# Kernel optimization log

Hardware: AMD Instinct MI355X
Metric: run time of the kernel (lower is better)

Reference implementation:

```python
import jax, jax.numpy as jnp
import numpy as np

D_MODEL = 2048
D_STATE = 16
D_CONV = 4
EXPAND = 2
D_INNER = EXPAND * D_MODEL  # 4096
DT_RANK = 128               # ceil(2048/16)
BATCH = 2
SEQ = 1024


def setup_inputs() -> dict:
    key = jax.random.key(0)
    ks = jax.random.split(key, 10)
    n = lambda k, shape, scale: jax.random.normal(k, shape, dtype=jnp.float32) * scale
    # A_log = log(arange(1..N)) broadcast over channels, exactly as in the torch init
    A_log = jnp.log(jnp.tile(jnp.arange(1, D_STATE + 1, dtype=jnp.float32)[None, :], (D_INNER, 1)))
    return {
        "hidden_states": n(ks[0], (BATCH, SEQ, D_MODEL), 1.0),
        "W_in": n(ks[1], (2 * D_INNER, D_MODEL), 0.02),
        "conv_w": n(ks[2], (D_INNER, D_CONV), 0.2),
        "conv_b": n(ks[3], (D_INNER,), 0.02),
        "W_x": n(ks[4], (DT_RANK + 2 * D_STATE, D_INNER), 0.02),
        "W_dt": n(ks[5], (D_INNER, DT_RANK), 0.05),
        "b_dt": n(ks[6], (D_INNER,), 0.5) - 4.0,  # softplus(b_dt) ~ small dt, like inv-softplus init
        "A_log": A_log,
        "D_skip": jnp.ones((D_INNER,), jnp.float32),
        "W_out": n(ks[7], (D_MODEL, D_INNER), 0.02),
    }


def _mamba_forward(hidden_states, W_in, conv_w, conv_b, W_x, W_dt, b_dt, A_log, D_skip, W_out):
    B, L, _ = hidden_states.shape
    # in_proj then split into x (SSM path) and z (gate)
    xz = hidden_states @ W_in.T                      # (B, L, 2*Di)
    x, z = jnp.split(xz, 2, axis=-1)                 # (B, L, Di) each
    # causal depthwise conv1d (kernel D_CONV, left pad D_CONV-1) + SiLU
    xp = jnp.pad(x, ((0, 0), (D_CONV - 1, 0), (0, 0)))
    xc = conv_b
    for k in range(D_CONV):
        xc = xc + conv_w[:, k] * xp[:, k:k + L, :]
    x = jax.nn.silu(xc)                              # (B, L, Di)
    # input-dependent dt, B, C
    x_dbl = x @ W_x.T                                # (B, L, dt_rank + 2N)
    dt_low, B_in, C_in = jnp.split(x_dbl, [DT_RANK, DT_RANK + D_STATE], axis=-1)
    dt = dt_low @ W_dt.T                             # (B, L, Di); bias added inside scan (delta_bias)
    delta = jax.nn.softplus(dt + b_dt)               # (B, L, Di)
    A = -jnp.exp(A_log)                              # (Di, N)

    def step(h, inp):
        delta_t, u_t, B_t, C_t = inp                 # (B,Di),(B,Di),(B,N),(B,N)
        dA = jnp.exp(delta_t[..., None] * A)         # (B, Di, N)
        h = dA * h + (delta_t * u_t)[..., None] * B_t[:, None, :]
        y_t = jnp.einsum('bdn,bn->bd', h, C_t)
        return h, y_t

    h0 = jnp.zeros((B, D_INNER, D_STATE), x.dtype)
    xs = (jnp.swapaxes(delta, 0, 1), jnp.swapaxes(x, 0, 1),
          jnp.swapaxes(B_in, 0, 1), jnp.swapaxes(C_in, 0, 1))
    _, ys = jax.lax.scan(step, h0, xs)               # ys: (L, B, Di)
    y = jnp.swapaxes(ys, 0, 1)                       # (B, L, Di)
    y = y + D_skip * x                               # skip connection
    y = y * jax.nn.silu(z)                           # output gating
    return y @ W_out.T                               # (B, L, D_MODEL)


def reference(hidden_states, W_in, conv_w, conv_b, W_x, W_dt, b_dt, A_log, D_skip, W_out):
    return _mamba_forward(hidden_states, W_in, conv_w, conv_b, W_x, W_dt, b_dt, A_log, D_skip, W_out)
```

## Files before the change

### kernel.cpp

```cpp
#include <hip/hip_runtime.h>
#include <hip/hip_bf16.h>


#define BATCH 2
#define SEQ 1024
#define DMODEL 2048
#define DINNER 4096
#define DSTATE 16
#define DTRANK 128
#define ROWS (BATCH * SEQ)
#define XDBL_N (DTRANK + 2 * DSTATE)
#define NCHUNK 64
#define CLEN (SEQ / NCHUNK)
#define WXPAD 192

typedef unsigned short ushort_t;
typedef __attribute__((ext_vector_type(8))) short short8;
typedef __attribute__((ext_vector_type(4))) float f32x4;

__device__ __forceinline__ ushort_t bf16_rne(float f) {
  unsigned u = __float_as_uint(f);
  return (ushort_t)((u + 0x7FFFu + ((u >> 16) & 1u)) >> 16);
}

__global__ __launch_bounds__(256) void cast_bf16(
    const float* __restrict__ x, ushort_t* __restrict__ o, int n4) {
  int i = blockIdx.x * 256 + threadIdx.x;
  if (i >= n4) return;
  float4 v = ((const float4*)x)[i];
  ushort4 h;
  h.x = bf16_rne(v.x); h.y = bf16_rne(v.y);
  h.z = bf16_rne(v.z); h.w = bf16_rne(v.w);
  ((ushort4*)o)[i] = h;
}

__global__ __launch_bounds__(256) void cast_wx(
    const float* __restrict__ wx, ushort_t* __restrict__ o) {
  int i = blockIdx.x * 256 + threadIdx.x;
  if (i >= WXPAD * (DINNER / 4)) return;
  int row = i >> 10;
  ushort4 h = {0, 0, 0, 0};
  if (row < XDBL_N) {
    float4 v = ((const float4*)wx)[i];
    h.x = bf16_rne(v.x); h.y = bf16_rne(v.y);
    h.z = bf16_rne(v.z); h.w = bf16_rne(v.w);
  }
  ((ushort4*)o)[i] = h;
}

template <int TM, int TN, int EPI, bool SK>
__global__ __launch_bounds__(256, 2) void gemm_bf16(
    const ushort_t* __restrict__ X, int lda,
    const ushort_t* __restrict__ W, int ldb,
    const float* __restrict__ bias,
    float* __restrict__ C, int ldc, int kslice, size_t sstride) {
  constexpr int MI = TM / 32;
  constexpr int NI = TN / 32;
  constexpr int G = (TM + TN) / 32;
  __shared__ __attribute__((aligned(16))) ushort_t lds[(TM + TN) * 64];

  const int tid = threadIdx.x;
  const int lane = tid & 63;
  const int w = tid >> 6;
  const int wm = w & 1, wn = w >> 1;
  const int m0 = blockIdx.x * TM;
  const int n0 = blockIdx.y * TN;
  const int kbase = SK ? blockIdx.z * kslice : 0;

  const int lrow = lane >> 3;
  const int csw = (lane & 7) ^ lrow;
  const int quad = lane >> 4;
  const int l15 = lane & 15;
  const int x0 = quad ^ (lane & 7);
  const int baseA = (wm * (TM / 2) + l15) * 64;
  const int baseB = (TM + wn * (TN / 2) + l15) * 64;

  f32x4 acc[MI][NI] = {};

  for (int kt = 0; kt < kslice; kt += 64) {
#pragma unroll
    for (int j = 0; j < G; j++) {
      const int r0 = (w * G + j) * 8;
      const int row = r0 + lrow;
      const ushort_t* src = (r0 < TM)
          ? X + (size_t)(m0 + row) * lda + kbase + kt + csw * 8
          : W + (size_t)(n0 + row - TM) * ldb + kbase + kt + csw * 8;
      __builtin_amdgcn_global_load_lds(
          (const __attribute__((address_space(1))) unsigned int*)src,
          (__attribute__((address_space(3))) unsigned int*)&lds[r0 * 64],
          16, 0, 0);
    }
    __syncthreads();

#pragma unroll
    for (int ks = 0; ks < 2; ks++) {
      const int xo = (x0 ^ (ks * 4)) * 8;
      short8 a[MI], b[NI];
#pragma unroll
      for (int mi = 0; mi < MI; mi++)
        a[mi] = *(const short8*)&lds[baseA + mi * 1024 + xo];
#pragma unroll
      for (int ni = 0; ni < NI; ni++)
        b[ni] = *(const short8*)&lds[baseB + ni * 1024 + xo];
#pragma unroll
      for (int mi = 0; mi < MI; mi++)
#pragma unroll
        for (int ni = 0; ni < NI; ni++)
          acc[mi][ni] = __builtin_amdgcn_mfma_f32_16x16x32_bf16(
              a[mi], b[ni], acc[mi][ni], 0, 0, 0);
    }
    __syncthreads();
  }

  float* Cs = SK ? (C + (size_t)blockIdx.z * sstride) : C;
#pragma unroll
  for (int mi = 0; mi < MI; mi++)
#pragma unroll
    for (int ni = 0; ni < NI; ni++) {
      int row = m0 + wm * (TM / 2) + mi * 16 + quad * 4;
      int col = n0 + wn * (TN / 2) + ni * 16 + l15;
#pragma unroll
      for (int r = 0; r < 4; r++) {
        float v = acc[mi][ni][r];
        if (EPI == 1) {
          v += bias[col];
          v = (v > 20.f) ? v : log1pf(__expf(v));
        }
        Cs[(size_t)(row + r) * ldc + col] = v;
      }
    }
}

__global__ __launch_bounds__(192) void reduce8(
    const float* __restrict__ partials, float* __restrict__ xdbl,
    ushort_t* __restrict__ dtb) {
  int m = blockIdx.x;
  int c = threadIdx.x;
  if (c >= XDBL_N) return;
  float s = 0.f;
#pragma unroll
  for (int z = 0; z < 8; z++)
    s += partials[(size_t)z * ROWS * WXPAD + (size_t)m * WXPAD + c];
  xdbl[(size_t)m * XDBL_N + c] = s;
  if (c < DTRANK) dtb[(size_t)m * DTRANK + c] = bf16_rne(s);
}

__global__ __launch_bounds__(256) void conv_silu(
    const float* __restrict__ xz, const float* __restrict__ cw,
    const float* __restrict__ cb, float* __restrict__ xs,
    ushort_t* __restrict__ xsb) {
  int idx = blockIdx.x * 256 + threadIdx.x;
  if (idx >= ROWS * DINNER) return;
  int d = idx & (DINNER - 1);
  int bt = idx >> 12;
  int t = bt & (SEQ - 1);
  float acc = cb[d];
#pragma unroll
  for (int k = 0; k < 4; k++) {
    int tt = t - 3 + k;
    if (tt >= 0) acc += cw[d * 4 + k] * xz[(size_t)(bt - 3 + k) * (2 * DINNER) + d];
  }
  float s = acc / (1.f + __expf(-acc));
  xs[idx] = s;
  xsb[idx] = bf16_rne(s);
}

__global__ __launch_bounds__(256) void scan_pass1(
    const float* __restrict__ delta, const float* __restrict__ xs,
    const float* __restrict__ xdbl, const float* __restrict__ A_log,
    float* __restrict__ hpart, float* __restrict__ sumd) {
  int g = blockIdx.x * 256 + threadIdx.x;
  int d = g & (DINNER - 1);
  int rest = g >> 12;
  int c = rest & (NCHUNK - 1);
  int b = rest >> 6;

  float Adn[16];
#pragma unroll
  for (int q = 0; q < 4; q++) {
    float4 a = *(const float4*)&A_log[d * 16 + q * 4];
    Adn[q * 4 + 0] = -__expf(a.x); Adn[q * 4 + 1] = -__expf(a.y);
    Adn[q * 4 + 2] = -__expf(a.z); Adn[q * 4 + 3] = -__expf(a.w);
  }

  float h[16] = {};
  float sd = 0.f;
  const size_t t0 = (size_t)b * SEQ + c * CLEN;
  const float* dp = delta + t0 * DINNER + d;
  const float* up = xs + t0 * DINNER + d;
  const float* xb = xdbl + t0 * XDBL_N + DTRANK;

  for (int i = 0; i < CLEN; i++) {
    float dt = dp[(size_t)i * DINNER];
    float u = up[(size_t)i * DINNER];
    sd += dt;
    float du = dt * u;
    float Bv[16];
#pragma unroll
    for (int q = 0; q < 4; q++)
      *(float4*)&Bv[q * 4] = *(const float4*)&xb[i * XDBL_N + q * 4];
#pragma unroll
    for (int n = 0; n < 16; n++)
      h[n] = __expf(dt * Adn[n]) * h[n] + du * Bv[n];
  }

  float* hp = hpart + ((size_t)(c * BATCH + b) * DINNER + d) * 16;
#pragma unroll
  for (int q = 0; q < 4; q++) *(float4*)&hp[q * 4] = *(const float4*)&h[q * 4];
  sumd[(size_t)(c * BATCH + b) * DINNER + d] = sd;
}

__global__ __launch_bounds__(256) void scan_pass2(
    float* __restrict__ hph, const float* __restrict__ sumd,
    const float* __restrict__ A_log) {
  int g = blockIdx.x * 256 + threadIdx.x;
  int n = g & 15;
  int d = (g >> 4) & (DINNER - 1);
  int b = g >> 16;

  float Adn = -__expf(A_log[d * 16 + n]);
  float h = 0.f;
  for (int c = 0; c < NCHUNK; c++) {
    size_t base = (size_t)(c * BATCH + b) * DINNER + d;
    float part = hph[base * 16 + n];
    hph[base * 16 + n] = h;
    h = __expf(Adn * sumd[base]) * h + part;
  }
}

__global__ __launch_bounds__(256) void scan_pass3(
    const float* __restrict__ xz, const float* __restrict__ xs,
    const float* __restrict__ xdbl, const float* __restrict__ A_log,
    const float* __restrict__ D_skip, const float* __restrict__ h0,
    const float* __restrict__ delta, ushort_t* __restrict__ gated) {
  int g = blockIdx.x * 256 + threadIdx.x;
  int d = g & (DINNER - 1);
  int rest = g >> 12;
  int c = rest & (NCHUNK - 1);
  int b = rest >> 6;

  float Adn[16];
#pragma unroll
  for (int q = 0; q < 4; q++) {
    float4 a = *(const float4*)&A_log[d * 16 + q * 4];
    Adn[q * 4 + 0] = -__expf(a.x); Adn[q * 4 + 1] = -__expf(a.y);
    Adn[q * 4 + 2] = -__expf(a.z); Adn[q * 4 + 3] = -__expf(a.w);
  }
  float Dd = D_skip[d];

  float h[16];
  const float* hp = h0 + ((size_t)(c * BATCH + b) * DINNER + d) * 16;
#pragma unroll
  for (int q = 0; q < 4; q++) *(float4*)&h[q * 4] = *(const float4*)&hp[q * 4];

  const size_t t0 = (size_t)b * SEQ + c * CLEN;
  const float* dl = delta + t0 * DINNER + d;
  const float* up = xs + t0 * DINNER + d;
  const float* zb = xz + t0 * (2 * DINNER) + DINNER + d;
  const float* xb = xdbl + t0 * XDBL_N + DTRANK;
  ushort_t* gp = gated + t0 * DINNER + d;

  for (int i = 0; i < CLEN; i++) {
    float dt = dl[(size_t)i * DINNER];
    float u = up[(size_t)i * DINNER];
    float du = dt * u;
    float Bv[16], Cv[16];
#pragma unroll
    for (int q = 0; q < 4; q++) {
      *(float4*)&Bv[q * 4] = *(const float4*)&xb[i * XDBL_N + q * 4];
      *(float4*)&Cv[q * 4] = *(const float4*)&xb[i * XDBL_N + DSTATE + q * 4];
    }
    float y = 0.f;
#pragma unroll
    for (int n = 0; n < 16; n++) {
      h[n] = __expf(dt * Adn[n]) * h[n] + du * Bv[n];
      y += h[n] * Cv[n];
    }
    float z = zb[(size_t)i * (2 * DINNER)];
    float sz = z / (1.f + __expf(-z));
    gp[(size_t)i * DINNER] = bf16_rne((y + Dd * u) * sz);
  }
}

extern "C" void kernel_launch(void* const* d_in, const int* in_sizes, int n_in,
                              void* d_out, int out_size, void* d_ws, size_t ws_size,
                              hipStream_t stream) {
  const float* hidden = (const float*)d_in[0];
  const float* W_in   = (const float*)d_in[1];
  const float* conv_w = (const float*)d_in[2];
  const float* conv_b = (const float*)d_in[3];
  const float* W_x    = (const float*)d_in[4];
  const float* W_dt   = (const float*)d_in[5];
  const float* b_dt   = (const float*)d_in[6];
  const float* A_log  = (const float*)d_in[7];
  const float* D_skip = (const float*)d_in[8];
  const float* W_out  = (const float*)d_in[9];
  float* out = (float*)d_out;

  float* ws    = (float*)d_ws;
  float* xz    = ws;
  float* xs    = xz + (size_t)ROWS * 2 * DINNER;
  float* xdbl  = xs + (size_t)ROWS * DINNER;
  float* delta = xdbl + (size_t)ROWS * XDBL_N;
  float* sumd  = delta + (size_t)ROWS * DINNER;
  float* hph   = sumd + (size_t)BATCH * DINNER * NCHUNK;
  ushort_t* Hb   = (ushort_t*)(hph + (size_t)BATCH * DINNER * NCHUNK * DSTATE);
  ushort_t* Wb1  = Hb + (size_t)ROWS * DMODEL;
  ushort_t* Wxb  = Wb1 + (size_t)2 * DINNER * DMODEL;
  ushort_t* Wdtb = Wxb + (size_t)WXPAD * DINNER;
  ushort_t* xsb  = Wdtb + (size_t)DINNER * DTRANK;
  ushort_t* dtb  = xsb + (size_t)ROWS * DINNER;
  float* partials = (float*)Wb1;
  ushort_t* Woutb = Wb1;
  ushort_t* gatedb = Wb1 + (size_t)DMODEL * DINNER;

  dim3 blk(256);

  cast_bf16<<<(ROWS * DMODEL / 4 + 255) / 256, blk, 0, stream>>>(
      hidden, Hb, ROWS * DMODEL / 4);
  cast_bf16<<<(2 * DINNER * DMODEL / 4 + 255) / 256, blk, 0, stream>>>(
      W_in, Wb1, 2 * DINNER * DMODEL / 4);

  gemm_bf16<128, 256, 0, false><<<dim3(16, 32), blk, 0, stream>>>(
      Hb, DMODEL, Wb1, DMODEL, nullptr, xz, 2 * DINNER, DMODEL, 0);

  conv_silu<<<(ROWS * DINNER + 255) / 256, blk, 0, stream>>>(
      xz, conv_w, conv_b, xs, xsb);

  cast_wx<<<(WXPAD * DINNER / 4 + 255) / 256, blk, 0, stream>>>(W_x, Wxb);
  cast_bf16<<<(DINNER * DTRANK / 4 + 255) / 256, blk, 0, stream>>>(
      W_dt, Wdtb, DINNER * DTRANK / 4);

  gemm_bf16<128, 64, 0, true><<<dim3(16, 3, 8), blk, 0, stream>>>(
      xsb, DINNER, Wxb, DINNER, nullptr, partials, WXPAD, DINNER / 8,
      (size_t)ROWS * WXPAD);
  reduce8<<<ROWS, dim3(WXPAD), 0, stream>>>(partials, xdbl, dtb);

  gemm_bf16<128, 128, 1, false><<<dim3(16, 32), blk, 0, stream>>>(
      dtb, DTRANK, Wdtb, DTRANK, b_dt, delta, DINNER, DTRANK, 0);

  scan_pass1<<<(BATCH * DINNER * NCHUNK) / 256, blk, 0, stream>>>(
      delta, xs, xdbl, A_log, hph, sumd);
  scan_pass2<<<(BATCH * DINNER * DSTATE) / 256, blk, 0, stream>>>(
      hph, sumd, A_log);
  scan_pass3<<<(BATCH * DINNER * NCHUNK) / 256, blk, 0, stream>>>(
      xz, xs, xdbl, A_log, D_skip, hph, delta, gatedb);

  cast_bf16<<<(DMODEL * DINNER / 4 + 255) / 256, blk, 0, stream>>>(
      W_out, Woutb, DMODEL * DINNER / 4);

  gemm_bf16<128, 128, 0, false><<<dim3(16, 16), blk, 0, stream>>>(
      gatedb, DINNER, Woutb, DINNER, nullptr, out, DMODEL, DINNER, 0);
}
```

Baseline: 481.7 us.

## Add 256x256 pipelined in_proj GEMM, vectorize conv_silu, halve scan chunks

Replaces the in_proj GEMM with a new 512-thread 256x256 tile kernel. It uses direct global-to-LDS loads, double buffering, interleaved MFMA clusters with priority hints, and a swizzled LDS layout, aiming for more data reuse and better overlap of memory and compute. The conv+SiLU kernel now processes four channels per thread with float4 loads and stores. The scan chunk count drops from 64 to 32, which gives the serial pass2 fewer steps but makes each pass1/pass3 thread longer and launches fewer threads.

```diff
diff --git a/kernel.cpp b/kernel.cpp
--- a/kernel.cpp
+++ b/kernel.cpp
@@ -10,7 +10,8 @@
 #define DTRANK 128
 #define ROWS (BATCH * SEQ)
 #define XDBL_N (DTRANK + 2 * DSTATE)
-#define NCHUNK 64
+#define NCHUNK 32
+#define LOG2_NCHUNK 5
 #define CLEN (SEQ / NCHUNK)
 #define WXPAD 192
 
@@ -131,6 +132,168 @@
     }
 }
 
+__device__ __forceinline__ void bar() {
+  asm volatile("" ::: "memory");
+  __builtin_amdgcn_s_barrier();
+  asm volatile("" ::: "memory");
+}
+#define VMWAIT(n) asm volatile("s_waitcnt vmcnt(" #n ")" ::: "memory")
+
+#define CLUSTER(AF, BF, MH, NH)                                           \
+  do {                                                                    \
+    __builtin_amdgcn_s_setprio(1);                                        \
+    _Pragma("unroll")                                                     \
+    for (int mi = 0; mi < 4; mi++)                                        \
+      _Pragma("unroll")                                                   \
+      for (int ni = 0; ni < 2; ni++)                                      \
+        _Pragma("unroll")                                                 \
+        for (int ks = 0; ks < 2; ks++)                                    \
+          acc[(MH) * 4 + mi][(NH) * 2 + ni] =                             \
+              __builtin_amdgcn_mfma_f32_16x16x32_bf16(                    \
+                  AF[mi][ks], BF[ni][ks],                                 \
+                  acc[(MH) * 4 + mi][(NH) * 2 + ni], 0, 0, 0);            \
+    __builtin_amdgcn_s_setprio(0);                                        \
+  } while (0)
+
+__global__ __launch_bounds__(512, 2) void gemm256(
+    const ushort_t* __restrict__ X, int lda,
+    const ushort_t* __restrict__ W, int ldb,
+    float* __restrict__ C, int ldc, int K) {
+  __shared__ __attribute__((aligned(16))) ushort_t lds[65536];
+  const int tid = threadIdx.x;
+  const int lane = tid & 63;
+  const int w = tid >> 6;
+  const int wm = w >> 2, wn = w & 3;
+  const int m0 = blockIdx.x * 256;
+  const int n0 = blockIdx.y * 256;
+  const int lrow = lane >> 3;
+  const int csw = (lane & 7) ^ lrow;
+  const int quad = lane >> 4;
+  const int l15 = lane & 15;
+  const int sx = lane & 7;
+
+  f32x4 acc[8][4] = {};
+  short8 a[4][2], b0[2][2], b1[2][2];
+
+  const ushort_t* Asrc = X + (size_t)(m0 + w * 8 + lrow) * lda + csw * 8;
+  const ushort_t* Bsrc = W + (size_t)(n0 + w * 8 + lrow) * ldb + csw * 8;
+
+  auto stA = [&](int buf, int g, int kt) {
+    __builtin_amdgcn_global_load_lds(
+        (const __attribute__((address_space(1))) unsigned int*)
+            (Asrc + (size_t)g * 64 * lda + kt),
+        (__attribute__((address_space(3))) unsigned int*)
+            &lds[buf * 16384 + (g * 64 + w * 8) * 64],
+        16, 0, 0);
+  };
+  auto stB = [&](int buf, int g, int kt) {
+    __builtin_amdgcn_global_load_lds(
+        (const __attribute__((address_space(1))) unsigned int*)
+            (Bsrc + (size_t)g * 64 * ldb + kt),
+        (__attribute__((address_space(3))) unsigned int*)
+            &lds[32768 + buf * 16384 + (g * 64 + w * 8) * 64],
+        16, 0, 0);
+  };
+  auto rdA = [&](int buf, int half, int mi, int ks) {
+    int row = wm * 128 + half * 64 + mi * 16 + l15;
+    int ch = (ks * 4 + quad) ^ sx;
+    return *(const short8*)&lds[buf * 16384 + row * 64 + ch * 8];
+  };
+  auto rdB = [&](int buf, int nh, int ni, int ks) {
+    int row = wn * 64 + nh * 32 + ni * 16 + l15;
+    int ch = (ks * 4 + quad) ^ sx;
+    return *(const short8*)&lds[32768 + buf * 16384 + row * 64 + ch * 8];
+  };
+
+#pragma unroll
+  for (int g = 0; g < 4; g++) stA(0, g, 0);
+#pragma unroll
+  for (int g = 0; g < 4; g++) stB(0, g, 0);
+  VMWAIT(0);
+  bar();
+
+  const int NT = K / 64;
+  int cur = 0;
+  for (int t = 0; t < NT - 1; ++t) {
+    const int nxt = cur ^ 1;
+    const int k2 = (t + 1) * 64;
+#pragma unroll
+    for (int mi = 0; mi < 4; mi++)
+#pragma unroll
+      for (int ks = 0; ks < 2; ks++) a[mi][ks] = rdA(cur, 0, mi, ks);
+#pragma unroll
+    for (int ni = 0; ni < 2; ni++)
+#pragma unroll
+      for (int ks = 0; ks < 2; ks++) b0[ni][ks] = rdB(cur, 0, ni, ks);
+    stB(nxt, 0, k2); stB(nxt, 1, k2);
+    bar();
+    CLUSTER(a, b0, 0, 0);
+    bar();
+#pragma unroll
+    for (int ni = 0; ni < 2; ni++)
+#pragma unroll
+      for (int ks = 0; ks < 2; ks++) b1[ni][ks] = rdB(cur, 1, ni, ks);
+    stB(nxt, 2, k2); stB(nxt, 3, k2);
+    bar();
+    CLUSTER(a, b1, 0, 1);
+    VMWAIT(4);
+    bar();
+#pragma unroll
+    for (int mi = 0; mi < 4; mi++)
+#pragma unroll
+      for (int ks = 0; ks < 2; ks++) a[mi][ks] = rdA(cur, 1, mi, ks);
+    stA(nxt, 0, k2); stA(nxt, 2, k2);
+    bar();
+    CLUSTER(a, b1, 1, 1);
+    bar();
+    stA(nxt, 1, k2); stA(nxt, 3, k2);
+    bar();
+    CLUSTER(a, b0, 1, 0);
+    VMWAIT(2);
+    bar();
+    cur = nxt;
+  }
+  {
+#pragma unroll
+    for (int mi = 0; mi < 4; mi++)
+#pragma unroll
+      for (int ks = 0; ks < 2; ks++) a[mi][ks] = rdA(cur, 0, mi, ks);
+#pragma unroll
+    for (int ni = 0; ni < 2; ni++)
+#pragma unroll
+      for (int ks = 0; ks < 2; ks++) b0[ni][ks] = rdB(cur, 0, ni, ks);
+    bar();
+    CLUSTER(a, b0, 0, 0);
+    bar();
+#pragma unroll
+    for (int ni = 0; ni < 2; ni++)
+#pragma unroll
+      for (int ks = 0; ks < 2; ks++) b1[ni][ks] = rdB(cur, 1, ni, ks);
+    bar();
+    CLUSTER(a, b1, 0, 1);
+    VMWAIT(0);
+    bar();
+#pragma unroll
+    for (int mi = 0; mi < 4; mi++)
+#pragma unroll
+      for (int ks = 0; ks < 2; ks++) a[mi][ks] = rdA(cur, 1, mi, ks);
+    bar();
+    CLUSTER(a, b1, 1, 1);
+    CLUSTER(a, b0, 1, 0);
+  }
+
+#pragma unroll
+  for (int mi = 0; mi < 8; mi++)
+#pragma unroll
+    for (int ni = 0; ni < 4; ni++) {
+      int row = m0 + wm * 128 + mi * 16 + quad * 4;
+      int col = n0 + wn * 64 + ni * 16 + l15;
+#pragma unroll
+      for (int r = 0; r < 4; r++)
+        C[(size_t)(row + r) * ldc + col] = acc[mi][ni][r];
+    }
+}
+
 __global__ __launch_bounds__(192) void reduce8(
     const float* __restrict__ partials, float* __restrict__ xdbl,
     ushort_t* __restrict__ dtb) {
@@ -150,19 +313,34 @@
     const float* __restrict__ cb, float* __restrict__ xs,
     ushort_t* __restrict__ xsb) {
   int idx = blockIdx.x * 256 + threadIdx.x;
-  if (idx >= ROWS * DINNER) return;
-  int d = idx & (DINNER - 1);
-  int bt = idx >> 12;
+  if (idx >= ROWS * DINNER / 4) return;
+  int d4 = idx & (DINNER / 4 - 1);
+  int bt = idx >> 10;
   int t = bt & (SEQ - 1);
-  float acc = cb[d];
+  int d = d4 * 4;
+  float4 c4 = *(const float4*)&cb[d];
+  float a0 = c4.x, a1 = c4.y, a2 = c4.z, a3 = c4.w;
 #pragma unroll
   for (int k = 0; k < 4; k++) {
     int tt = t - 3 + k;
-    if (tt >= 0) acc += cw[d * 4 + k] * xz[(size_t)(bt - 3 + k) * (2 * DINNER) + d];
-  }
-  float s = acc / (1.f + __expf(-acc));
-  xs[idx] = s;
-  xsb[idx] = bf16_rne(s);
+    if (tt >= 0) {
+      float4 v = *(const float4*)&xz[(size_t)(bt - 3 + k) * (2 * DINNER) + d];
+      a0 += cw[(d + 0) * 4 + k] * v.x;
+      a1 += cw[(d + 1) * 4 + k] * v.y;
+      a2 += cw[(d + 2) * 4 + k] * v.z;
+      a3 += cw[(d + 3) * 4 + k] * v.w;
+    }
+  }
+  float4 s;
+  s.x = a0 / (1.f + __expf(-a0));
+  s.y = a1 / (1.f + __expf(-a1));
+  s.z = a2 / (1.f + __expf(-a2));
+  s.w = a3 / (1.f + __expf(-a3));
+  *(float4*)&xs[(size_t)bt * DINNER + d] = s;
+  ushort4 h;
+  h.x = bf16_rne(s.x); h.y = bf16_rne(s.y);
+  h.z = bf16_rne(s.z); h.w = bf16_rne(s.w);
+  *(ushort4*)&xsb[(size_t)bt * DINNER + d] = h;
 }
 
 __global__ __launch_bounds__(256) void scan_pass1(
@@ -173,7 +351,7 @@
   int d = g & (DINNER - 1);
   int rest = g >> 12;
   int c = rest & (NCHUNK - 1);
-  int b = rest >> 6;
+  int b = rest >> LOG2_NCHUNK;
 
   float Adn[16];
 #pragma unroll
@@ -237,7 +415,7 @@
   int d = g & (DINNER - 1);
   int rest = g >> 12;
   int c = rest & (NCHUNK - 1);
-  int b = rest >> 6;
+  int b = rest >> LOG2_NCHUNK;
 
   float Adn[16];
 #pragma unroll
@@ -321,10 +499,10 @@
   cast_bf16<<<(2 * DINNER * DMODEL / 4 + 255) / 256, blk, 0, stream>>>(
       W_in, Wb1, 2 * DINNER * DMODEL / 4);
 
-  gemm_bf16<128, 256, 0, false><<<dim3(16, 32), blk, 0, stream>>>(
-      Hb, DMODEL, Wb1, DMODEL, nullptr, xz, 2 * DINNER, DMODEL, 0);
-
-  conv_silu<<<(ROWS * DINNER + 255) / 256, blk, 0, stream>>>(
+  gemm256<<<dim3(8, 32), dim3(512), 0, stream>>>(
+      Hb, DMODEL, Wb1, DMODEL, xz, 2 * DINNER, DMODEL);
+
+  conv_silu<<<(ROWS * DINNER / 4 + 255) / 256, blk, 0, stream>>>(
       xz, conv_w, conv_b, xs, xsb);
 
   cast_wx<<<(WXPAD * DINNER / 4 + 255) / 256, blk, 0, stream>>>(W_x, Wxb);
```

Result: slower. 500.7 us (+3.9%).
